# Kernel tuning notes

Measured on AMD Instinct MI355X. Metric: run time of the kernel, lower is better.

Reference implementation:

```python
import jax, jax.numpy as jnp
import numpy as np

B, T, E, V, L, BLK = 2, 2048, 1024, 32000, 12, 2048


def setup_inputs() -> dict:
    key = jax.random.key(0)
    ks = jax.random.split(key, 10)
    std = 0.005  # FHE-friendly tiny init, matches nn.init.normal_(std=0.005)
    init = lambda k, shape: jax.random.normal(k, shape, jnp.float32) * std
    return {
        "idx": jax.random.randint(ks[0], (B, T), 0, V, dtype=jnp.int32),
        "wte": init(ks[1], (V, E)),
        "wpe": init(ks[2], (BLK, E)),
        "ln1_w": jnp.ones((L, E), jnp.float32),   # FHELayerNorm weights init to ones
        "Wq": init(ks[3], (L, E, E)),
        "Wk": init(ks[4], (L, E, E)),
        "Wv": init(ks[5], (L, E, E)),
        "Wo": init(ks[6], (L, E, E)),
        "ln2_w": jnp.ones((L, E), jnp.float32),
        "fc1": init(ks[7], (L, 2 * E, E)),
        "fc2": init(ks[8], (L, E, 2 * E)),
        "lnf_w": jnp.ones((E,), jnp.float32),
        "lm_head": init(ks[9], (V, E)),
    }


def reference(idx, wte, wpe, ln1_w, Wq, Wk, Wv, Wo, ln2_w, fc1, fc2, lnf_w, lm_head):
    t = idx.shape[1]
    # embeddings, each scaled by 0.01
    x = wte[idx] * 0.01 + (wpe[:t] * 0.01)[None, :, :]  # [B,T,E]

    n_layer = ln1_w.shape[0]
    # inter-block rescale: 0.1 after every block except the last
    scales = jnp.where(jnp.arange(n_layer) < n_layer - 1, 0.1, 1.0).astype(x.dtype)

    def block(x, p):
        ln1, wq, wk, wv, wo, ln2, f1, f2, s = p
        # FHELayerNorm: pure scaling
        h = x * ln1 * 0.1
        # attention (single head over full E, softmax-free quadratic weights)
        q = jnp.einsum('bte,fe->btf', h, wq) * 0.01
        k = jnp.einsum('bte,fe->btf', h, wk) * 0.01
        v = jnp.einsum('bte,fe->btf', h, wv) * 0.1
        a = jnp.einsum('btf,bsf->bts', q, k) * 0.01      # [B,T,T]
        a = a * a * 0.1 + a * 0.1                         # pointwise quadratic
        ao = jnp.einsum('bts,bsf->btf', a, v) * 0.01
        attn_out = jnp.einsum('btf,ef->bte', ao, wo) * 0.1
        x = (x * 0.5 + attn_out * 0.5) * 0.1
        # MLP with polynomial activation
        h2 = x * ln2 * 0.1
        m = jnp.einsum('bte,fe->btf', h2, f1) * 0.05      # [B,T,2E]
        m = m * m * 0.1 + m * 0.1
        m = jnp.einsum('btf,ef->bte', m, f2) * 0.05
        x = (x * 0.5 + m * 0.5) * 0.1
        return x * s, None

    x, _ = jax.lax.scan(block, x, (ln1_w, Wq, Wk, Wv, Wo, ln2_w, fc1, fc2, scales))
    x = x * lnf_w * 0.1  # final FHELayerNorm
    logits = jnp.einsum('bte,ve->btv', x, lm_head) * 0.5
    return logits
```

## Files before the change

### kernel.cpp

```cpp
#include <hip/hip_runtime.h>
#include <hip/hip_fp8.h>
#include <stdint.h>
#include <math.h>

typedef unsigned short u16;
typedef __attribute__((ext_vector_type(8))) short bf16x8;
typedef __attribute__((ext_vector_type(4))) float f32x4;
typedef __attribute__((ext_vector_type(2))) long long llx2;

typedef __attribute__((address_space(1))) const uint32_t gas_u32;
typedef __attribute__((address_space(3))) uint32_t las_u32;

__device__ __forceinline__ u16 f2b(float f) {
  union { float f; uint32_t u; } v; v.f = f;
  uint32_t r = v.u + 0x7FFFu + ((v.u >> 16) & 1u);
  return (u16)(r >> 16);
}
__device__ __forceinline__ float b2f(u16 b) {
  union { uint32_t u; float f; } v; v.u = ((uint32_t)b) << 16; return v.f;
}
__device__ __forceinline__ uint8_t f8(float x) {
  __hip_fp8_e4m3 t(x);
  return (uint8_t)t.__x;
}
__device__ __forceinline__ int ipos(int k) {
  return (k & ~63) | (k & 7) | ((k & 32) >> 2) | ((k & 24) << 1);
}

__device__ __forceinline__ void gl_lds16(const void* g, void* l) {
  __builtin_amdgcn_global_load_lds((gas_u32*)g, (las_u32*)l, 16, 0, 0);
}
__device__ __forceinline__ void barrier_raw() {
  asm volatile("" ::: "memory");
  __builtin_amdgcn_s_barrier();
  asm volatile("" ::: "memory");
}

#define MM(A_, B_, C_)  __builtin_amdgcn_mfma_f32_16x16x32_bf16(A_, B_, C_, 0, 0, 0)
#define MM8(A_, B_, C_) __builtin_amdgcn_mfma_f32_16x16x32_fp8_fp8(A_, B_, C_, 0, 0, 0)

struct GP {
  const u16* A; long long asb;
  const u16* B[3]; long long bsb;
  u16* O[3]; long long osb;
  int M, N, K, lda, ldb, ldo;
  float alpha[3];
  int epi[3];
  int nsel, msel;
  float* fout; int ldf;
};

template <int MI>
__device__ __forceinline__ void epi_store(const GP& p, u16* __restrict__ Op, float alpha, int epi,
                                          int rbase0, int colb, const f32x4 (&acc)[MI][4], int l4, int l15) {
#pragma unroll
  for (int mi = 0; mi < MI; ++mi) {
    const int rbase = rbase0 + mi * 16 + l4 * 4;
#pragma unroll
    for (int ni = 0; ni < 4; ++ni) {
      const int col = colb + ni * 16 + l15;
      f32x4 v = acc[mi][ni];
#pragma unroll
      for (int r = 0; r < 4; ++r)
        Op[(size_t)(rbase + r) * p.ldo + col] = f2b(v[r] * alpha);
    }
  }
}

__device__ __forceinline__ void xcd_swz(int nwg, int orig, int gx, int& bx, int& by) {
  const int xcd = orig & 7, rem = orig >> 3;
  const int qq = nwg >> 3, rr = nwg & 7;
  const int wg = (xcd < rr ? xcd * (qq + 1) : rr * (qq + 1) + (xcd - rr) * qq) + rem;
  bx = wg % gx; by = wg / gx;
}

#define RD_A(off) do { \
  a0 = *(const bf16x8*)(Abase + (off));        a1 = *(const bf16x8*)(Abase + (off) + 1024); \
  a2 = *(const bf16x8*)(Abase + (off) + 2048); a3 = *(const bf16x8*)(Abase + (off) + 3072); \
} while (0)
#define RD_B(off) do { \
  b0 = *(const bf16x8*)(Bbase + (off));        b1 = *(const bf16x8*)(Bbase + (off) + 1024); \
  b2 = *(const bf16x8*)(Bbase + (off) + 2048); b3 = *(const bf16x8*)(Bbase + (off) + 3072); \
} while (0)
#define MF16(R) do { \
  acc[R+0][0]=MM(a0,b0,acc[R+0][0]); acc[R+0][1]=MM(a0,b1,acc[R+0][1]); acc[R+0][2]=MM(a0,b2,acc[R+0][2]); acc[R+0][3]=MM(a0,b3,acc[R+0][3]); \
  acc[R+1][0]=MM(a1,b0,acc[R+1][0]); acc[R+1][1]=MM(a1,b1,acc[R+1][1]); acc[R+1][2]=MM(a1,b2,acc[R+1][2]); acc[R+1][3]=MM(a1,b3,acc[R+1][3]); \
  acc[R+2][0]=MM(a2,b0,acc[R+2][0]); acc[R+2][1]=MM(a2,b1,acc[R+2][1]); acc[R+2][2]=MM(a2,b2,acc[R+2][2]); acc[R+2][3]=MM(a2,b3,acc[R+2][3]); \
  acc[R+3][0]=MM(a3,b0,acc[R+3][0]); acc[R+3][1]=MM(a3,b1,acc[R+3][1]); acc[R+3][2]=MM(a3,b2,acc[R+3][2]); acc[R+3][3]=MM(a3,b3,acc[R+3][3]); \
} while (0)

#define PHASE_MID() do { \
  asm volatile("s_waitcnt lgkmcnt(0)" ::: "memory"); \
  __builtin_amdgcn_sched_barrier(0); \
  __builtin_amdgcn_s_setprio(1); \
} while (0)
#define PHASE_END() do { \
  __builtin_amdgcn_s_setprio(0); \
  __builtin_amdgcn_sched_barrier(0); \
  barrier_raw(); \
} while (0)

#define SSA(q, kh, t) do { \
  gl_lds16(gA0 + (size_t)(t) * 64 + (kh) * 32, lAw + (q) * 32768 + (kh) * 8192); \
  gl_lds16(gA1 + (size_t)(t) * 64 + (kh) * 32, lAw + (q) * 32768 + (kh) * 8192 + 4096); \
} while (0)
#define SSB(q, kh, t) do { \
  gl_lds16(gB0 + (size_t)(t) * 64 + (kh) * 32, lBw + (q) * 32768 + (kh) * 8192); \
  gl_lds16(gB1 + (size_t)(t) * 64 + (kh) * 32, lBw + (q) * 32768 + (kh) * 8192 + 4096); \
} while (0)

__global__ __launch_bounds__(256, 2) void gemmS_k(GP p) {
  extern __shared__ __attribute__((aligned(16))) char lds[];
  const int z = blockIdx.z;
  int bx, by;
  xcd_swz(gridDim.x * gridDim.y, blockIdx.y * gridDim.x + blockIdx.x, gridDim.x, bx, by);
  const int m0 = bx * 128, n0 = by * 128;
  const u16* __restrict__ Ap = p.A + (size_t)z * p.asb;
  const u16* __restrict__ Bp = p.B[0] + (size_t)z * p.bsb;

  const int tid = threadIdx.x, wid = tid >> 6, lane = tid & 63;
  const int wm = wid >> 1, wn = wid & 1;
  const int l15 = lane & 15, l4 = lane >> 4;
  const int cswz16 = (l4 ^ ((l15 >> 1) & 3)) * 16;

  const f32x4 vzero = {0.f, 0.f, 0.f, 0.f};
  f32x4 acc[4][4];
#pragma unroll
  for (int i = 0; i < 4; ++i)
#pragma unroll
    for (int j = 0; j < 4; ++j) acc[i][j] = vzero;

  const int sr = lane >> 2;
  const int cg8 = ((lane & 3) ^ ((lane >> 3) & 3)) * 8;
  const u16* gA0 = Ap + (size_t)(m0 + wid * 16 + sr) * p.lda + cg8;
  const u16* gA1 = gA0 + (size_t)64 * p.lda;
  const u16* gB0 = Bp + (size_t)(n0 + wid * 16 + sr) * p.ldb + cg8;
  const u16* gB1 = gB0 + (size_t)64 * p.ldb;
  char* lAw = lds + wid * 1024;
  char* lBw = lds + 16384 + wid * 1024;

  const int nt = p.K >> 6;

  SSA(0, 0, 0); SSB(0, 0, 0); SSA(0, 1, 0); SSB(0, 1, 0);
  SSA(1, 0, 1); SSB(1, 0, 1);
  asm volatile("s_waitcnt vmcnt(4)" ::: "memory");
  barrier_raw();

  bf16x8 a0, a1, a2, a3, b0, b1, b2, b3;
  for (int t = 0; t < nt; ++t) {
    const int q = t & 1;
    const char* Abase = lds + q * 32768 + (wm * 64 + l15) * 64 + cswz16;
    const char* Bbase = lds + q * 32768 + 16384 + (wn * 64 + l15) * 64 + cswz16;
    RD_A(0); RD_B(0);
    if (t + 1 < nt) { SSA(q ^ 1, 1, t + 1); SSB(q ^ 1, 1, t + 1); }
    PHASE_MID(); MF16(0); PHASE_END();
    RD_A(8192); RD_B(8192);
    if (t + 2 < nt) { SSA(q, 0, t + 2); SSB(q, 0, t + 2); }
    PHASE_MID(); MF16(0);
    __builtin_amdgcn_s_setprio(0);
    __builtin_amdgcn_sched_barrier(0);
    if (t + 2 < nt) asm volatile("s_waitcnt vmcnt(4)" ::: "memory");
    else            asm volatile("s_waitcnt vmcnt(0)" ::: "memory");
    barrier_raw();
  }

  u16* Op = p.O[0] + (size_t)z * p.osb;
  epi_store<4>(p, Op, p.alpha[0], p.epi[0], m0 + wm * 64, n0 + wn * 64, acc, l4, l15);
}

struct GP8 {
  const uint8_t* A; long long asb;
  const uint8_t* B[3]; long long bsb;
  uint8_t* O[3]; long long osb;
  int K, lda, ldb, ldo;
  float m1[3], m2[3];
  int epi[3];
  int nsel, msel, nfirst;
  float qc;
  float* xres; const float* lnw; float rscale; float oscale;
  uint8_t* h8out;
  float* fout; int ldf;
};

#define S8A(q, kh, t) do { \
  gl_lds16(gA0 + (size_t)(t) * 128 + (kh) * 64, lAw + (q) * 32768 + (kh) * 8192); \
  gl_lds16(gA1 + (size_t)(t) * 128 + (kh) * 64, lAw + (q) * 32768 + (kh) * 8192 + 4096); \
} while (0)
#define S8B(q, kh, t) do { \
  gl_lds16(gB0 + (size_t)(t) * 128 + (kh) * 64, lBw + (q) * 32768 + (kh) * 8192); \
  gl_lds16(gB1 + (size_t)(t) * 128 + (kh) * 64, lBw + (q) * 32768 + (kh) * 8192 + 4096); \
} while (0)

#define MF8() do { \
  acc[0][0]=MM8(a0[0],b0[0],acc[0][0]); acc[0][0]=MM8(a0[1],b0[1],acc[0][0]); \
  acc[0][1]=MM8(a0[0],b1[0],acc[0][1]); acc[0][1]=MM8(a0[1],b1[1],acc[0][1]); \
  acc[0][2]=MM8(a0[0],b2[0],acc[0][2]); acc[0][2]=MM8(a0[1],b2[1],acc[0][2]); \
  acc[0][3]=MM8(a0[0],b3[0],acc[0][3]); acc[0][3]=MM8(a0[1],b3[1],acc[0][3]); \
  acc[1][0]=MM8(a1[0],b0[0],acc[1][0]); acc[1][0]=MM8(a1[1],b0[1],acc[1][0]); \
  acc[1][1]=MM8(a1[0],b1[0],acc[1][1]); acc[1][1]=MM8(a1[1],b1[1],acc[1][1]); \
  acc[1][2]=MM8(a1[0],b2[0],acc[1][2]); acc[1][2]=MM8(a1[1],b2[1],acc[1][2]); \
  acc[1][3]=MM8(a1[0],b3[0],acc[1][3]); acc[1][3]=MM8(a1[1],b3[1],acc[1][3]); \
  acc[2][0]=MM8(a2[0],b0[0],acc[2][0]); acc[2][0]=MM8(a2[1],b0[1],acc[2][0]); \
  acc[2][1]=MM8(a2[0],b1[0],acc[2][1]); acc[2][1]=MM8(a2[1],b1[1],acc[2][1]); \
  acc[2][2]=MM8(a2[0],b2[0],acc[2][2]); acc[2][2]=MM8(a2[1],b2[1],acc[2][2]); \
  acc[2][3]=MM8(a2[0],b3[0],acc[2][3]); acc[2][3]=MM8(a2[1],b3[1],acc[2][3]); \
  acc[3][0]=MM8(a3[0],b0[0],acc[3][0]); acc[3][0]=MM8(a3[1],b0[1],acc[3][0]); \
  acc[3][1]=MM8(a3[0],b1[0],acc[3][1]); acc[3][1]=MM8(a3[1],b1[1],acc[3][1]); \
  acc[3][2]=MM8(a3[0],b2[0],acc[3][2]); acc[3][2]=MM8(a3[1],b2[1],acc[3][2]); \
  acc[3][3]=MM8(a3[0],b3[0],acc[3][3]); acc[3][3]=MM8(a3[1],b3[1],acc[3][3]); \
} while (0)

__global__ __launch_bounds__(256, 2) void gemm8_k(GP8 p) {
  extern __shared__ __attribute__((aligned(16))) char lds[];
  const int z = blockIdx.z;
  int bx, by;
  xcd_swz(gridDim.x * gridDim.y, blockIdx.y * gridDim.x + blockIdx.x, gridDim.x, bx, by);
  const int m0 = p.nfirst ? by * 128 : bx * 128;
  const int n0 = p.nfirst ? bx * 128 : by * 128;
  const int zi = p.nsel ? (n0 >> 10) : 0;
  const int nB = p.nsel ? (n0 & 1023) : n0;
  const uint8_t* __restrict__ Ap = p.A + (size_t)z * p.asb;
  const uint8_t* __restrict__ Bp = p.B[zi] + (size_t)(p.msel ? (m0 >> 11) : z) * p.bsb;

  const int tid = threadIdx.x, wid = tid >> 6, lane = tid & 63;
  const int wm = wid >> 1, wn = wid & 1;
  const int l15 = lane & 15, l4 = lane >> 4;
  const int cswz16 = (l4 ^ ((l15 >> 1) & 3)) * 16;

  const f32x4 vzero = {0.f, 0.f, 0.f, 0.f};
  f32x4 acc[4][4];
#pragma unroll
  for (int i = 0; i < 4; ++i)
#pragma unroll
    for (int j = 0; j < 4; ++j) acc[i][j] = vzero;

  const int sr = lane >> 2;
  const int cgB = ((lane & 3) ^ ((lane >> 3) & 3)) * 16;
  const uint8_t* gA0 = Ap + (size_t)(m0 + wid * 16 + sr) * p.lda + cgB;
  const uint8_t* gA1 = gA0 + (size_t)64 * p.lda;
  const uint8_t* gB0 = Bp + (size_t)(nB + wid * 16 + sr) * p.ldb + cgB;
  const uint8_t* gB1 = gB0 + (size_t)64 * p.ldb;
  char* lAw = lds + wid * 1024;
  char* lBw = lds + 16384 + wid * 1024;

  const int nt = p.K >> 7;

  S8A(0, 0, 0); S8B(0, 0, 0); S8A(0, 1, 0); S8B(0, 1, 0);
  S8A(1, 0, 1); S8B(1, 0, 1);
  asm volatile("s_waitcnt vmcnt(4)" ::: "memory");
  barrier_raw();

  llx2 a0, a1, a2, a3, b0, b1, b2, b3;
  for (int t = 0; t < nt; ++t) {
    const int q = t & 1;
    const char* Abase = lds + q * 32768 + (wm * 64 + l15) * 64 + cswz16;
    const char* Bbase = lds + q * 32768 + 16384 + (wn * 64 + l15) * 64 + cswz16;
    a0 = *(const llx2*)Abase;          a1 = *(const llx2*)(Abase + 1024);
    a2 = *(const llx2*)(Abase + 2048); a3 = *(const llx2*)(Abase + 3072);
    b0 = *(const llx2*)Bbase;          b1 = *(const llx2*)(Bbase + 1024);
    b2 = *(const llx2*)(Bbase + 2048); b3 = *(const llx2*)(Bbase + 3072);
    if (t + 1 < nt) { S8A(q ^ 1, 1, t + 1); S8B(q ^ 1, 1, t + 1); }
    PHASE_MID(); MF8(); PHASE_END();
    a0 = *(const llx2*)(Abase + 8192);        a1 = *(const llx2*)(Abase + 8192 + 1024);
    a2 = *(const llx2*)(Abase + 8192 + 2048); a3 = *(const llx2*)(Abase + 8192 + 3072);
    b0 = *(const llx2*)(Bbase + 8192);        b1 = *(const llx2*)(Bbase + 8192 + 1024);
    b2 = *(const llx2*)(Bbase + 8192 + 2048); b3 = *(const llx2*)(Bbase + 8192 + 3072);
    if (t + 2 < nt) { S8A(q, 0, t + 2); S8B(q, 0, t + 2); }
    PHASE_MID(); MF8();
    __builtin_amdgcn_s_setprio(0);
    __builtin_amdgcn_sched_barrier(0);
    if (t + 2 < nt) asm volatile("s_waitcnt vmcnt(4)" ::: "memory");
    else            asm volatile("s_waitcnt vmcnt(0)" ::: "memory");
    barrier_raw();
  }

  const int epi = p.epi[zi];
  const float m1v = p.m1[zi], m2v = p.m2[zi];
  uint8_t* __restrict__ Op = p.O[zi] + (size_t)z * p.osb;
#pragma unroll
  for (int mi = 0; mi < 4; ++mi) {
    const int rbase = m0 + wm * 64 + mi * 16 + l4 * 4;
#pragma unroll
    for (int ni = 0; ni < 4; ++ni) {
      const int col = nB + wn * 64 + ni * 16 + l15;
      f32x4 v = acc[mi][ni];
      if (epi == 0) {
#pragma unroll
        for (int r = 0; r < 4; ++r) {
          float y = (v[r] * m1v) * m2v;
          Op[(size_t)(rbase + r) * p.ldo + ipos(col)] = f8(y);
        }
      } else if (epi == 1) {
        const int b = rbase >> 11, rb = rbase & 2047;
        uint32_t pk = 0;
#pragma unroll
        for (int r = 0; r < 4; ++r) {
          float y = (v[r] * m1v) * m2v;
          pk |= (uint32_t)f8(y) << (8 * r);
        }
        *(uint32_t*)(Op + (size_t)b * 2097152 + (size_t)col * 2048 + ipos(rb)) = pk;
      } else if (epi == 2) {
#pragma unroll
        for (int r = 0; r < 4; ++r) {
          float u = (v[r] * m1v) * m2v;
          Op[(size_t)(rbase + r) * p.ldo + ipos(col)] = f8(u * u * p.qc + u);
        }
      } else if (epi == 3) {
#pragma unroll
        for (int r = 0; r < 4; ++r) {
          float add = (v[r] * m1v) * m2v;
          size_t ix = (size_t)(rbase + r) * 1024 + col;
          float xn = (p.xres[ix] + add) * p.rscale;
          p.xres[ix] = xn;
          float hv = xn * p.lnw[col] * 0.1f;
          p.h8out[(size_t)(rbase + r) * 1024 + ipos(col)] = f8(hv * p.oscale);
        }
      } else {
#pragma unroll
        for (int r = 0; r < 4; ++r)
          __builtin_nontemporal_store((v[r] * m1v) * m2v,
                                      &p.fout[(size_t)(rbase + r) * p.ldf + col]);
      }
    }
  }
}

__global__ __launch_bounds__(256) void embed8_k(const int* __restrict__ idx, const float* __restrict__ wte,
                                                const float* __restrict__ wpe, const float* __restrict__ ln1,
                                                float* __restrict__ x, uint8_t* __restrict__ h8, float sh) {
  const int bt = blockIdx.x;
  const int t = bt & 2047;
  const int tok = idx[bt];
  const int e = threadIdx.x * 4;
  const float4 wv = *(const float4*)(wte + (size_t)tok * 1024 + e);
  const float4 pv = *(const float4*)(wpe + (size_t)t * 1024 + e);
  const float4 lv = *(const float4*)(ln1 + e);
  float4 xo;
  xo.x = (wv.x + pv.x) * 0.01f;
  xo.y = (wv.y + pv.y) * 0.01f;
  xo.z = (wv.z + pv.z) * 0.01f;
  xo.w = (wv.w + pv.w) * 0.01f;
  *(float4*)(x + (size_t)bt * 1024 + e) = xo;
  uint32_t pk = (uint32_t)f8(xo.x * lv.x * 0.1f * sh)
              | ((uint32_t)f8(xo.y * lv.y * 0.1f * sh) << 8)
              | ((uint32_t)f8(xo.z * lv.z * 0.1f * sh) << 16)
              | ((uint32_t)f8(xo.w * lv.w * 0.1f * sh) << 24);
  *(uint32_t*)(h8 + (size_t)bt * 1024 + ipos(e)) = pk;
}

__global__ __launch_bounds__(256) void cvt_k(const float* __restrict__ src, u16* __restrict__ dst, long long n) {
  long long i = ((long long)blockIdx.x * 256 + threadIdx.x) * 8;
  const long long stride = (long long)gridDim.x * 256 * 8;
  for (; i < n; i += stride) {
    const float4 a = *(const float4*)(src + i);
    const float4 b = *(const float4*)(src + i + 4);
    bf16x8 o;
    o[0] = (short)f2b(a.x); o[1] = (short)f2b(a.y); o[2] = (short)f2b(a.z); o[3] = (short)f2b(a.w);
    o[4] = (short)f2b(b.x); o[5] = (short)f2b(b.y); o[6] = (short)f2b(b.z); o[7] = (short)f2b(b.w);
    *(bf16x8*)(dst + i) = o;
  }
}

__global__ __launch_bounds__(256) void cvtT_k(const float* __restrict__ src, u16* __restrict__ dst) {
  __shared__ float tl[64][68];
  const int z = blockIdx.z;
  const int c0 = blockIdx.x * 64, r0 = blockIdx.y * 64;
  const int tid = threadIdx.x;
  const float* s = src + (size_t)z * 1048576;
#pragma unroll
  for (int it = 0; it < 4; ++it) {
    const int r = it * 16 + (tid >> 4);
    const int c4 = (tid & 15) * 4;
    const float4 v = *(const float4*)(s + (size_t)(r0 + r) * 1024 + c0 + c4);
    tl[r][c4] = v.x; tl[r][c4 + 1] = v.y; tl[r][c4 + 2] = v.z; tl[r][c4 + 3] = v.w;
  }
  __syncthreads();
  const int c = tid >> 2;
  const int rr = (tid & 3) * 16;
  u16* d = dst + (size_t)z * 1048576 + (size_t)(c0 + c) * 1024 + r0 + rr;
  bf16x8 o0, o1;
#pragma unroll
  for (int j = 0; j < 8; ++j) o0[j] = (short)f2b(tl[rr + j][c]);
#pragma unroll
  for (int j = 0; j < 8; ++j) o1[j] = (short)f2b(tl[rr + 8 + j][c]);
  *(bf16x8*)d = o0;
  *(bf16x8*)(d + 8) = o1;
}

__global__ __launch_bounds__(256) void cvt8i_k(const u16* __restrict__ src, uint8_t* __restrict__ dst,
                                               long long n, float scale) {
  long long i = ((long long)blockIdx.x * 256 + threadIdx.x) * 8;
  const long long stride = (long long)gridDim.x * 256 * 8;
  for (; i < n; i += stride) {
    const bf16x8 v = *(const bf16x8*)(src + i);
    uint32_t lo = 0, hi = 0;
#pragma unroll
    for (int j = 0; j < 4; ++j) lo |= (uint32_t)f8(b2f((u16)v[j]) * scale) << (8 * j);
#pragma unroll
    for (int j = 0; j < 4; ++j) hi |= (uint32_t)f8(b2f((u16)v[4 + j]) * scale) << (8 * j);
    uint8_t* d = dst + ((i & ~63ll) | (((i >> 3) & 3) << 4) | (((i >> 5) & 1) << 3));
    *(uint32_t*)d = lo;
    *(uint32_t*)(d + 4) = hi;
  }
}

__global__ __launch_bounds__(256) void cvtf8i_k(const float* __restrict__ src, uint8_t* __restrict__ dst,
                                                long long n, float scale) {
  long long i = ((long long)blockIdx.x * 256 + threadIdx.x) * 8;
  const long long stride = (long long)gridDim.x * 256 * 8;
  for (; i < n; i += stride) {
    const float4 a = *(const float4*)(src + i);
    const float4 b = *(const float4*)(src + i + 4);
    uint32_t lo = (uint32_t)f8(a.x * scale) | ((uint32_t)f8(a.y * scale) << 8)
                | ((uint32_t)f8(a.z * scale) << 16) | ((uint32_t)f8(a.w * scale) << 24);
    uint32_t hi = (uint32_t)f8(b.x * scale) | ((uint32_t)f8(b.y * scale) << 8)
                | ((uint32_t)f8(b.z * scale) << 16) | ((uint32_t)f8(b.w * scale) << 24);
    uint8_t* d = dst + ((i & ~63ll) | (((i >> 3) & 3) << 4) | (((i >> 5) & 1) << 3));
    *(uint32_t*)d = lo;
    *(uint32_t*)(d + 4) = hi;
  }
}

__global__ __launch_bounds__(256) void megacvt8_k(const float* __restrict__ wq, const float* __restrict__ wk,
                                                  const float* __restrict__ f1, const float* __restrict__ f2,
                                                  uint8_t* __restrict__ dst, float scale) {
  const long long M1 = 1ll << 20;
  const long long per = 6 * M1;
  const long long total = 12 * per;
  long long i = ((long long)blockIdx.x * 256 + threadIdx.x) * 8;
  const long long stride = (long long)gridDim.x * 256 * 8;
  for (; i < total; i += stride) {
    const long long l = i / per;
    const long long off = i - l * per;
    const float* s; long long so;
    if      (off < M1)     { s = wq; so = l * M1 + off; }
    else if (off < 2 * M1) { s = wk; so = l * M1 + off - M1; }
    else if (off < 4 * M1) { s = f1; so = l * 2 * M1 + off - 2 * M1; }
    else                   { s = f2; so = l * 2 * M1 + off - 4 * M1; }
    const float4 a = *(const float4*)(s + so);
    const float4 b = *(const float4*)(s + so + 4);
    uint32_t lo = (uint32_t)f8(a.x * scale) | ((uint32_t)f8(a.y * scale) << 8)
                | ((uint32_t)f8(a.z * scale) << 16) | ((uint32_t)f8(a.w * scale) << 24);
    uint32_t hi = (uint32_t)f8(b.x * scale) | ((uint32_t)f8(b.y * scale) << 8)
                | ((uint32_t)f8(b.z * scale) << 16) | ((uint32_t)f8(b.w * scale) << 24);
    uint8_t* d = dst + ((i & ~63ll) | (((i >> 3) & 3) << 4) | (((i >> 5) & 1) << 3));
    *(uint32_t*)d = lo;
    *(uint32_t*)(d + 4) = hi;
  }
}

static inline double scp(double sigma) {
  double e = round(log2(0.5 / sigma));
  if (e > 120.0) e = 120.0;
  if (e < -120.0) e = -120.0;
  return ldexp(1.0, (int)e);
}
static inline void split2(double v, float& a, float& b) {
  if (v == 0.0) { a = 0.f; b = 0.f; return; }
  int e; frexp(v, &e);
  int h = e / 2;
  a = (float)ldexp(1.0, h);
  b = (float)ldexp(v, -h);
}

extern "C" void kernel_launch(void* const* d_in, const int* in_sizes, int n_in,
                              void* d_out, int out_size, void* d_ws, size_t ws_size,
                              hipStream_t stream) {
  const int*   idx  = (const int*)  d_in[0];
  const float* wte  = (const float*)d_in[1];
  const float* wpe  = (const float*)d_in[2];
  const float* ln1w = (const float*)d_in[3];
  const float* Wq   = (const float*)d_in[4];
  const float* Wk   = (const float*)d_in[5];
  const float* Wv   = (const float*)d_in[6];
  const float* Wo   = (const float*)d_in[7];
  const float* ln2w = (const float*)d_in[8];
  const float* fc1  = (const float*)d_in[9];
  const float* fc2  = (const float*)d_in[10];
  const float* lnfw = (const float*)d_in[11];
  const float* lmh  = (const float*)d_in[12];
  float* out = (float*)d_out;

  double dSh1[12], dSqk[12], dSaq[12], dSu[12], dSh2[12], dSmq[12], dShF;
  {
    double sx = 7e-5;
    for (int l = 0; l < 12; ++l) {
      double sh1 = sx * 0.1;
      double sq  = sh1 * 0.005 * 32.0 * 0.01;
      double saq = 32.0 * sq * sq * 0.01 * 0.1;
      double su  = sh1 * 8e-4 * 32.0 * 0.1;
      double sx2 = sx * 0.05;
      double sh2 = sx2 * 0.1;
      double smq = sh2 * 0.005 * 32.0 * 0.05 * 0.1;
      dSh1[l] = scp(sh1); dSqk[l] = scp(sq); dSaq[l] = scp(saq);
      dSu[l] = scp(su); dSh2[l] = scp(sh2); dSmq[l] = scp(smq);
      sx = sx2 * 0.05 * (l < 11 ? 0.1 : 1.0);
    }
    dShF = scp(sx * 0.1);
  }
  const double SW = 128.0, SWVO = 512.0, SF = 128.0, SL = 128.0;

  char* w = (char*)d_ws;
  float*   x    = (float*)w;    w += (size_t)4096 * 1024 * 4;
  uint8_t* h8   = (uint8_t*)w;  w += (size_t)4096 * 1024;
  uint8_t* q8   = (uint8_t*)w;  w += (size_t)4096 * 1024;
  uint8_t* k8   = (uint8_t*)w;  w += (size_t)4096 * 1024;
  uint8_t* uT8  = (uint8_t*)w;  w += (size_t)2 * 1024 * 2048;
  uint8_t* a8   = (uint8_t*)w;  w += (size_t)2 * 2048 * 2048;
  uint8_t* mb8  = (uint8_t*)w;  w += (size_t)4096 * 2048;
  uint8_t* lw8  = (uint8_t*)w;  w += (size_t)12 * 6291456;
  uint8_t* wvo8 = (uint8_t*)w;  w += (size_t)12 * 1048576;
  uint8_t* lmh8 = q8;
  u16* WvT   = (u16*)lw8;
  u16* WoB   = (u16*)(lw8 + 25165824);
  u16* Wvo16 = (u16*)(lw8 + 50331648);

  const size_t SHS = 65536, SH8 = 65536;

  embed8_k<<<4096, 256, 0, stream>>>(idx, wte, wpe, ln1w, x, h8, (float)dSh1[0]);

  cvtT_k<<<dim3(16, 16, 12), 256, 0, stream>>>(Wv, WvT);
  cvt_k<<<2048, 256, 0, stream>>>(Wo, WoB, 12ll * 1048576);
  {
    GP p{};
    p.A = WoB; p.asb = 1048576;
    p.B[0] = WvT; p.bsb = 1048576;
    p.O[0] = Wvo16; p.osb = 1048576;
    p.M = 1024; p.N = 1024; p.K = 1024; p.lda = 1024; p.ldb = 1024; p.ldo = 1024;
    p.alpha[0] = 1.0f; p.epi[0] = 0;
    gemmS_k<<<dim3(8, 8, 12), 256, SHS, stream>>>(p);
  }
  cvt8i_k<<<2048, 256, 0, stream>>>(Wvo16, wvo8, 12ll * 1048576, (float)SWVO);
  megacvt8_k<<<2048, 256, 0, stream>>>(Wq, Wk, fc1, fc2, lw8, (float)SW);

  for (int l = 0; l < 12; ++l) {
    uint8_t* lwl = lw8 + (size_t)l * 6291456;
    {
      GP8 p{};
      p.A = h8; p.asb = 0;
      p.B[0] = lwl; p.B[1] = lwl + 1048576; p.B[2] = wvo8 + (size_t)l * 1048576; p.bsb = 0;
      p.O[0] = q8; p.O[1] = k8; p.O[2] = uT8; p.osb = 0;
      p.K = 1024; p.lda = 1024; p.ldb = 1024; p.ldo = 1024;
      split2(0.01 * dSqk[l] / (dSh1[l] * SW), p.m1[0], p.m2[0]);
      p.m1[1] = p.m1[0]; p.m2[1] = p.m2[0];
      split2(0.1 * dSu[l] / (dSh1[l] * SWVO), p.m1[2], p.m2[2]);
      p.epi[0] = 0; p.epi[1] = 0; p.epi[2] = 1;
      p.nsel = 1;
      gemm8_k<<<dim3(32, 24, 1), 256, SH8, stream>>>(p);
    }
    {
      GP8 p{};
      p.A = q8; p.asb = 2097152;
      p.B[0] = k8; p.bsb = 2097152;
      p.O[0] = a8; p.osb = 4194304;
      p.K = 1024; p.lda = 1024; p.ldb = 1024; p.ldo = 2048;
      split2(0.001 * dSaq[l] / (dSqk[l] * dSqk[l]), p.m1[0], p.m2[0]);
      p.qc = (float)(10.0 / dSaq[l]);
      p.epi[0] = 2;
      gemm8_k<<<dim3(16, 16, 2), 256, SH8, stream>>>(p);
    }
    {
      GP8 p{};
      p.A = a8; p.asb = 0;
      p.B[0] = uT8; p.bsb = 2097152; p.msel = 1;
      p.O[0] = a8; p.osb = 0;
      p.K = 2048; p.lda = 2048; p.ldb = 2048; p.ldo = 1024;
      split2(0.001 / (dSaq[l] * dSu[l]), p.m1[0], p.m2[0]);
      p.epi[0] = 3;
      p.xres = x; p.lnw = ln2w + (size_t)l * 1024; p.rscale = 0.05f;
      p.oscale = (float)dSh2[l]; p.h8out = h8;
      gemm8_k<<<dim3(32, 8, 1), 256, SH8, stream>>>(p);
    }
    {
      GP8 p{};
      p.A = h8; p.asb = 0;
      p.B[0] = lwl + 2097152; p.bsb = 0;
      p.O[0] = mb8; p.osb = 0;
      p.K = 1024; p.lda = 1024; p.ldb = 1024; p.ldo = 2048;
      split2(0.005 * dSmq[l] / (dSh2[l] * SF), p.m1[0], p.m2[0]);
      p.qc = (float)(10.0 / dSmq[l]);
      p.epi[0] = 2;
      gemm8_k<<<dim3(32, 16, 1), 256, SH8, stream>>>(p);
    }
    {
      GP8 p{};
      p.A = mb8; p.asb = 0;
      p.B[0] = lwl + 4194304; p.bsb = 0;
      p.O[0] = mb8; p.osb = 0;
      p.K = 2048; p.lda = 2048; p.ldb = 2048; p.ldo = 1024;
      split2(0.05 / (dSmq[l] * SF), p.m1[0], p.m2[0]);
      p.epi[0] = 3;
      p.xres = x;
      p.rscale = (l < 11) ? 0.005f : 0.05f;
      if (l < 11) { p.lnw = ln1w + (size_t)(l + 1) * 1024; p.oscale = (float)dSh1[l + 1]; }
      else        { p.lnw = lnfw; p.oscale = (float)dShF; }
      p.h8out = h8;
      gemm8_k<<<dim3(32, 8, 1), 256, SH8, stream>>>(p);
    }
  }

  cvtf8i_k<<<2048, 256, 0, stream>>>(lmh, lmh8, 32768000ll, (float)SL);
  {
    GP8 p{};
    p.A = h8; p.asb = 0;
    p.B[0] = lmh8; p.bsb = 0;
    p.O[0] = lmh8; p.osb = 0;
    p.K = 1024; p.lda = 1024; p.ldb = 1024; p.ldo = 0;
    split2(0.5 / (dShF * SL), p.m1[0], p.m2[0]);
    p.epi[0] = 4;
    p.nfirst = 1;
    p.fout = out; p.ldf = 32000;
    gemm8_k<<<dim3(250, 32, 1), 256, SH8, stream>>>(p);
  }
}
```

Measured before the change: 2.215 ms.

## Add 64x128 triple-buffered FP8 GEMM kernel for per-layer matmuls

Introduces gemm8h_k, an FP8 MFMA GEMM with a 64x128 tile, triple-buffered LDS staging (two tiles in flight) and launch bounds of 2 blocks per CU. All five per-layer GEMMs switch to it with doubled grid x. The aim is more workgroups for these mid-sized matmuls, which should fill the CUs better and hide memory latency through deeper prefetch. The cost is lower per-block data reuse from the smaller M tile and more LDS per block.

```diff
diff --git a/kernel.cpp b/kernel.cpp
--- a/kernel.cpp
+++ b/kernel.cpp
@@ -280,6 +280,144 @@
 #pragma unroll
   for (int mi = 0; mi < 4; ++mi) {
     const int rbase = m0 + wm * 64 + mi * 16 + l4 * 4;
+#pragma unroll
+    for (int ni = 0; ni < 4; ++ni) {
+      const int col = nB + wn * 64 + ni * 16 + l15;
+      f32x4 v = acc[mi][ni];
+      if (epi == 0) {
+#pragma unroll
+        for (int r = 0; r < 4; ++r) {
+          float y = (v[r] * m1v) * m2v;
+          Op[(size_t)(rbase + r) * p.ldo + ipos(col)] = f8(y);
+        }
+      } else if (epi == 1) {
+        const int b = rbase >> 11, rb = rbase & 2047;
+        uint32_t pk = 0;
+#pragma unroll
+        for (int r = 0; r < 4; ++r) {
+          float y = (v[r] * m1v) * m2v;
+          pk |= (uint32_t)f8(y) << (8 * r);
+        }
+        *(uint32_t*)(Op + (size_t)b * 2097152 + (size_t)col * 2048 + ipos(rb)) = pk;
+      } else if (epi == 2) {
+#pragma unroll
+        for (int r = 0; r < 4; ++r) {
+          float u = (v[r] * m1v) * m2v;
+          Op[(size_t)(rbase + r) * p.ldo + ipos(col)] = f8(u * u * p.qc + u);
+        }
+      } else if (epi == 3) {
+#pragma unroll
+        for (int r = 0; r < 4; ++r) {
+          float add = (v[r] * m1v) * m2v;
+          size_t ix = (size_t)(rbase + r) * 1024 + col;
+          float xn = (p.xres[ix] + add) * p.rscale;
+          p.xres[ix] = xn;
+          float hv = xn * p.lnw[col] * 0.1f;
+          p.h8out[(size_t)(rbase + r) * 1024 + ipos(col)] = f8(hv * p.oscale);
+        }
+      } else {
+#pragma unroll
+        for (int r = 0; r < 4; ++r)
+          __builtin_nontemporal_store((v[r] * m1v) * m2v,
+                                      &p.fout[(size_t)(rbase + r) * p.ldf + col]);
+      }
+    }
+  }
+}
+
+#define H8STAGE(b, t) do { \
+  gl_lds16(gA0 + (size_t)(t) * 128,      lds + (b) * 24576 + wid * 1024); \
+  gl_lds16(gB0 + (size_t)(t) * 128,      lds + (b) * 24576 + 8192 + wid * 1024); \
+  gl_lds16(gB1 + (size_t)(t) * 128,      lds + (b) * 24576 + 12288 + wid * 1024); \
+  gl_lds16(gA0 + (size_t)(t) * 128 + 64, lds + (b) * 24576 + 4096 + wid * 1024); \
+  gl_lds16(gB0 + (size_t)(t) * 128 + 64, lds + (b) * 24576 + 16384 + wid * 1024); \
+  gl_lds16(gB1 + (size_t)(t) * 128 + 64, lds + (b) * 24576 + 20480 + wid * 1024); \
+} while (0)
+
+#define MF8H(AK, BK_) do { \
+  acc[0][0]=MM8(a0##AK[0],b0##BK_[0],acc[0][0]); acc[0][0]=MM8(a0##AK[1],b0##BK_[1],acc[0][0]); \
+  acc[0][1]=MM8(a0##AK[0],b1##BK_[0],acc[0][1]); acc[0][1]=MM8(a0##AK[1],b1##BK_[1],acc[0][1]); \
+  acc[0][2]=MM8(a0##AK[0],b2##BK_[0],acc[0][2]); acc[0][2]=MM8(a0##AK[1],b2##BK_[1],acc[0][2]); \
+  acc[0][3]=MM8(a0##AK[0],b3##BK_[0],acc[0][3]); acc[0][3]=MM8(a0##AK[1],b3##BK_[1],acc[0][3]); \
+  acc[1][0]=MM8(a1##AK[0],b0##BK_[0],acc[1][0]); acc[1][0]=MM8(a1##AK[1],b0##BK_[1],acc[1][0]); \
+  acc[1][1]=MM8(a1##AK[0],b1##BK_[0],acc[1][1]); acc[1][1]=MM8(a1##AK[1],b1##BK_[1],acc[1][1]); \
+  acc[1][2]=MM8(a1##AK[0],b2##BK_[0],acc[1][2]); acc[1][2]=MM8(a1##AK[1],b2##BK_[1],acc[1][2]); \
+  acc[1][3]=MM8(a1##AK[0],b3##BK_[0],acc[1][3]); acc[1][3]=MM8(a1##AK[1],b3##BK_[1],acc[1][3]); \
+} while (0)
+
+__global__ __launch_bounds__(256, 2) void gemm8h_k(GP8 p) {
+  extern __shared__ __attribute__((aligned(16))) char lds[];
+  const int z = blockIdx.z;
+  int bx, by;
+  xcd_swz(gridDim.x * gridDim.y, blockIdx.y * gridDim.x + blockIdx.x, gridDim.x, bx, by);
+  const int m0 = bx * 64, n0 = by * 128;
+  const int zi = p.nsel ? (n0 >> 10) : 0;
+  const int nB = p.nsel ? (n0 & 1023) : n0;
+  const uint8_t* __restrict__ Ap = p.A + (size_t)z * p.asb;
+  const uint8_t* __restrict__ Bp = p.B[zi] + (size_t)(p.msel ? (m0 >> 11) : z) * p.bsb;
+
+  const int tid = threadIdx.x, wid = tid >> 6, lane = tid & 63;
+  const int wm = wid >> 1, wn = wid & 1;
+  const int l15 = lane & 15, l4 = lane >> 4;
+  const int cswz16 = (l4 ^ ((l15 >> 1) & 3)) * 16;
+
+  const f32x4 vzero = {0.f, 0.f, 0.f, 0.f};
+  f32x4 acc[2][4];
+#pragma unroll
+  for (int i = 0; i < 2; ++i)
+#pragma unroll
+    for (int j = 0; j < 4; ++j) acc[i][j] = vzero;
+
+  const int sr = lane >> 2;
+  const int cgB = ((lane & 3) ^ ((lane >> 3) & 3)) * 16;
+  const uint8_t* gA0 = Ap + (size_t)(m0 + wid * 16 + sr) * p.lda + cgB;
+  const uint8_t* gB0 = Bp + (size_t)(nB + wid * 16 + sr) * p.ldb + cgB;
+  const uint8_t* gB1 = gB0 + (size_t)64 * p.ldb;
+
+  const int nt = p.K >> 7;
+
+  H8STAGE(0, 0);
+  H8STAGE(1, 1);
+  asm volatile("s_waitcnt vmcnt(6)" ::: "memory");
+  barrier_raw();
+
+  int q = 0;
+  for (int t = 0; t < nt; ++t) {
+    const int bn = (q == 0) ? 2 : q - 1;
+    const char* Abase = lds + q * 24576 + (wm * 32 + l15) * 64 + cswz16;
+    const char* Bbase = lds + q * 24576 + 8192 + (wn * 64 + l15) * 64 + cswz16;
+    llx2 a0k0 = *(const llx2*)Abase;
+    llx2 a1k0 = *(const llx2*)(Abase + 1024);
+    llx2 a0k1 = *(const llx2*)(Abase + 4096);
+    llx2 a1k1 = *(const llx2*)(Abase + 4096 + 1024);
+    llx2 b0k0 = *(const llx2*)Bbase;
+    llx2 b1k0 = *(const llx2*)(Bbase + 1024);
+    llx2 b2k0 = *(const llx2*)(Bbase + 2048);
+    llx2 b3k0 = *(const llx2*)(Bbase + 3072);
+    llx2 b0k1 = *(const llx2*)(Bbase + 8192);
+    llx2 b1k1 = *(const llx2*)(Bbase + 8192 + 1024);
+    llx2 b2k1 = *(const llx2*)(Bbase + 8192 + 2048);
+    llx2 b3k1 = *(const llx2*)(Bbase + 8192 + 3072);
+    if (t + 2 < nt) H8STAGE(bn, t + 2);
+    asm volatile("s_waitcnt lgkmcnt(0)" ::: "memory");
+    __builtin_amdgcn_sched_barrier(0);
+    __builtin_amdgcn_s_setprio(1);
+    MF8H(k0, k0);
+    MF8H(k1, k1);
+    __builtin_amdgcn_s_setprio(0);
+    __builtin_amdgcn_sched_barrier(0);
+    if (t + 2 < nt) asm volatile("s_waitcnt vmcnt(6)" ::: "memory");
+    else            asm volatile("s_waitcnt vmcnt(0)" ::: "memory");
+    barrier_raw();
+    q = (q == 2) ? 0 : q + 1;
+  }
+
+  const int epi = p.epi[zi];
+  const float m1v = p.m1[zi], m2v = p.m2[zi];
+  uint8_t* __restrict__ Op = p.O[zi] + (size_t)z * p.osb;
+#pragma unroll
+  for (int mi = 0; mi < 2; ++mi) {
+    const int rbase = m0 + wm * 32 + mi * 16 + l4 * 4;
 #pragma unroll
     for (int ni = 0; ni < 4; ++ni) {
       const int col = nB + wn * 64 + ni * 16 + l15;
@@ -515,7 +653,7 @@
   u16* WoB   = (u16*)(lw8 + 25165824);
   u16* Wvo16 = (u16*)(lw8 + 50331648);
 
-  const size_t SHS = 65536, SH8 = 65536;
+  const size_t SHS = 65536, SH8 = 65536, SHH = 73728;
 
   embed8_k<<<4096, 256, 0, stream>>>(idx, wte, wpe, ln1w, x, h8, (float)dSh1[0]);
 
@@ -546,7 +684,7 @@
       split2(0.1 * dSu[l] / (dSh1[l] * SWVO), p.m1[2], p.m2[2]);
       p.epi[0] = 0; p.epi[1] = 0; p.epi[2] = 1;
       p.nsel = 1;
-      gemm8_k<<<dim3(32, 24, 1), 256, SH8, stream>>>(p);
+      gemm8h_k<<<dim3(64, 24, 1), 256, SHH, stream>>>(p);
     }
     {
       GP8 p{};
@@ -557,7 +695,7 @@
       split2(0.001 * dSaq[l] / (dSqk[l] * dSqk[l]), p.m1[0], p.m2[0]);
       p.qc = (float)(10.0 / dSaq[l]);
       p.epi[0] = 2;
-      gemm8_k<<<dim3(16, 16, 2), 256, SH8, stream>>>(p);
+      gemm8h_k<<<dim3(32, 16, 2), 256, SHH, stream>>>(p);
     }
     {
       GP8 p{};
@@ -569,7 +707,7 @@
       p.epi[0] = 3;
       p.xres = x; p.lnw = ln2w + (size_t)l * 1024; p.rscale = 0.05f;
       p.oscale = (float)dSh2[l]; p.h8out = h8;
-      gemm8_k<<<dim3(32, 8, 1), 256, SH8, stream>>>(p);
+      gemm8h_k<<<dim3(64, 8, 1), 256, SHH, stream>>>(p);
     }
     {
       GP8 p{};
@@ -580,7 +718,7 @@
       split2(0.005 * dSmq[l] / (dSh2[l] * SF), p.m1[0], p.m2[0]);
       p.qc = (float)(10.0 / dSmq[l]);
       p.epi[0] = 2;
-      gemm8_k<<<dim3(32, 16, 1), 256, SH8, stream>>>(p);
+      gemm8h_k<<<dim3(64, 16, 1), 256, SHH, stream>>>(p);
     }
     {
       GP8 p{};
@@ -595,7 +733,7 @@
       if (l < 11) { p.lnw = ln1w + (size_t)(l + 1) * 1024; p.oscale = (float)dSh1[l + 1]; }
       else        { p.lnw = lnfw; p.oscale = (float)dShF; }
       p.h8out = h8;
-      gemm8_k<<<dim3(32, 8, 1), 256, SH8, stream>>>(p);
+      gemm8h_k<<<dim3(64, 8, 1), 256, SHH, stream>>>(p);
     }
   }
 
```

After: 2.110 ms. -4.7%, faster.
